# Performance work log

Hardware: AMD Instinct MI355X
Metric: run time of the kernel (lower is better)

The kernel has to match this reference:

```python
import jax, jax.numpy as jnp
import numpy as np

B, H, S, DH = 1, 16, 4096, 64
SPARSITY = 0.1
NEG = -1e9


def setup_inputs() -> dict:
    key = jax.random.key(0)
    kq, kk, kv, kp, km = jax.random.split(key, 5)
    query = jax.random.normal(kq, (B, H, S, DH), dtype=jnp.float32)
    k_ = jax.random.normal(kk, (B, H, S, DH), dtype=jnp.float32)
    v_ = jax.random.normal(kv, (B, H, S, DH), dtype=jnp.float32)
    pat = jax.random.uniform(kp, (S, S)) < SPARSITY
    pat = pat | jnp.eye(S, dtype=bool)
    sparse_pattern = pat[None, None]  # [1,1,S,S]
    mask = jax.random.randint(km, (1, 1, 1, S), 0, 2, dtype=jnp.int32)
    return {"query": query, "key": k_, "value": v_,
            "sparse_pattern": sparse_pattern, "mask": mask}


def reference(query, key, value, sparse_pattern, mask):
    scale = 1.0 / jnp.sqrt(jnp.asarray(DH, dtype=query.dtype))
    # [B,H,S,S] attention scores
    scores = jnp.einsum('bhqd,bhkd->bhqk', query, key) * scale
    scores = jnp.where(sparse_pattern, scores, NEG)
    scores = jnp.where(mask == 0, NEG, scores)
    weights = jax.nn.softmax(scores, axis=-1)
    return jnp.einsum('bhqk,bhkd->bhqd', weights, value)
```

## Files before the change

### kernel.cpp

```cpp
#include <hip/hip_runtime.h>
#include <hip/hip_bf16.h>

#define S_LEN 4096
#define DHD   64
#define NH    16
#define NKT   64
#define KVB   64
#define WQ    32
#define NW    4
#define QB    (WQ * NW)
#define QSCALE 0.18033688011112042f
#define THRS   8.656170245333781f

typedef __bf16 bf16x8 __attribute__((ext_vector_type(8)));
typedef __bf16 bf16x4 __attribute__((ext_vector_type(4)));
typedef float  f32x16 __attribute__((ext_vector_type(16)));
typedef float  f32x4  __attribute__((ext_vector_type(4)));
typedef unsigned u32;
typedef unsigned u32x4v __attribute__((ext_vector_type(4)));
typedef unsigned long long u64;

#define MFMA32 __builtin_amdgcn_mfma_f32_32x32x16_bf16

__device__ __forceinline__ float fexp2(float x) {
  float r;
  asm("v_exp_f32 %0, %1" : "=v"(r) : "v"(x));
  return r;
}
#define EXP2(x) fexp2(x)

__device__ __forceinline__ int swz(int row, int col) {
  return row * 64 + ((((col >> 3) ^ (row & 7)) << 3) | (col & 7));
}

__device__ __forceinline__ u32 pk(float a, float b) {
  __bf16 x = (__bf16)a, y = (__bf16)b;
  u32 lo = (u32)__builtin_bit_cast(unsigned short, x);
  u32 hi = (u32)__builtin_bit_cast(unsigned short, y);
  return lo | (hi << 16);
}

__device__ __forceinline__ void gload16(const void* g, void* l) {
  __builtin_amdgcn_global_load_lds((const __attribute__((address_space(1))) void*)g,
                                   (__attribute__((address_space(3))) void*)l, 16, 0, 0);
}

__device__ __forceinline__ void plswap(u32& x, u32& y) {
  asm("v_permlane32_swap_b32 %0, %1" : "+v"(x), "+v"(y));
}

union PAW { u32x4v w; bf16x8 h; };

template <int MODE>
__device__ __forceinline__ bool patget(const void* __restrict__ p, int q, int k) {
  const size_t idx = (size_t)q * S_LEN + k;
  if constexpr (MODE == 1) return ((const unsigned char*)p)[idx] != 0;
  else if constexpr (MODE == 0) return ((const int*)p)[idx] != 0;
  else return ((const float*)p)[idx] != 0.0f;
}

__global__ void __launch_bounds__(256, 2) attn32c(
    const float* __restrict__ Qg, const __bf16* __restrict__ Kc, const __bf16* __restrict__ Vc,
    const u64* __restrict__ packw,
    const int* __restrict__ mask, float* __restrict__ out) {
  __shared__ __align__(16) __bf16 Kls[4][KVB * DHD];
  __shared__ __align__(16) __bf16 Vls[4][DHD * KVB];
  __shared__ float sfb[NW][WQ];
  __shared__ int msum[NW];

  const int gid = (blockIdx.x & 7) * 64 + (blockIdx.x >> 3);
  const int h = gid >> 5;
  const int q0 = (gid & 31) * QB;

  const int t = threadIdx.x, lane = t & 63, wv = t >> 6;
  const int l32 = lane & 31, hi = lane >> 5;
  const int qrow = q0 + wv * WQ + l32;

  int c = 0;
#pragma unroll
  for (int j = 0; j < 16; j++) c += (mask[t * 16 + j] != 0);
#pragma unroll
  for (int d = 1; d < 64; d <<= 1) c += __shfl_xor(c, d);
  if (lane == 0) msum[wv] = c;

  bf16x8 aQ[4];
  {
    const float* qp = Qg + ((size_t)h * S_LEN + qrow) * DHD;
#pragma unroll
    for (int cc = 0; cc < 4; cc++) {
      float4 x = *(const float4*)(qp + cc * 16 + hi * 8);
      float4 y = *(const float4*)(qp + cc * 16 + hi * 8 + 4);
      bf16x8 f;
      f[0] = (__bf16)(x.x * QSCALE); f[1] = (__bf16)(x.y * QSCALE);
      f[2] = (__bf16)(x.z * QSCALE); f[3] = (__bf16)(x.w * QSCALE);
      f[4] = (__bf16)(y.x * QSCALE); f[5] = (__bf16)(y.y * QSCALE);
      f[6] = (__bf16)(y.z * QSCALE); f[7] = (__bf16)(y.w * QSCALE);
      aQ[cc] = f;
    }
  }
  bf16x8 onesf;
#pragma unroll
  for (int j = 0; j < 8; j++) onesf[j] = (__bf16)1.0f;
  f32x16 zv;
#pragma unroll
  for (int r = 0; r < 16; r++) zv[r] = 0.f;

  __syncthreads();
  const int nact = msum[0] + msum[1] + msum[2] + msum[3];
  const int nt = (nact + 63) >> 6;
  const int np = ((nt + 1) & ~1) >> 1;

  const __bf16* Kb = Kc + (size_t)h * NKT * 4096;
  const __bf16* Vb = Vc + (size_t)h * NKT * 4096;

  auto stage = [&](int slot, int kt) {
    const __bf16* kbase = Kb + (size_t)kt * 4096;
    const __bf16* vbase = Vb + (size_t)kt * 4096;
#pragma unroll
    for (int i = 0; i < 2; i++) {
      const int j = wv * 2 + i;
      gload16(kbase + j * 512 + lane * 8, &Kls[slot][j * 512]);
      gload16(vbase + j * 512 + lane * 8, &Vls[slot][j * 512]);
    }
  };

  f32x16 Oc0 = zv, Oc1 = zv, Ol = zv;
  float m_run = -__builtin_inff();
  const u64* prow = packw + qrow;

  __builtin_amdgcn_sched_barrier(0);
  u64 pwA = prow[0];
  u64 pwB = prow[(size_t)1 * S_LEN];
  stage(0, 0);
  stage(1, 1);

  for (int it = 0; it < np; it++) {
    const int buf = (it & 1) << 1;
    u64 pwA_n = 0, pwB_n = 0;
    if (it + 1 < np) {
      pwA_n = prow[(size_t)(2 * it + 2) * S_LEN];
      pwB_n = prow[(size_t)(2 * it + 3) * S_LEN];
      stage(buf ^ 2, 2 * it + 2);
      stage((buf ^ 2) + 1, 2 * it + 3);
      asm volatile("s_waitcnt vmcnt(10)" ::: "memory");
    } else {
      asm volatile("s_waitcnt vmcnt(0)" ::: "memory");
    }
    __builtin_amdgcn_s_barrier();
    __builtin_amdgcn_sched_barrier(0);

    const __bf16* KlA = Kls[buf];
    const __bf16* KlB = Kls[buf + 1];
    const __bf16* VlA = Vls[buf];
    const __bf16* VlB = Vls[buf + 1];

    f32x16 pA0, pA1, pB0, pB1;
    __builtin_amdgcn_s_setprio(1);
#pragma unroll
    for (int cc = 0; cc < 4; cc++) {
      const int g = (((2 * cc + hi) ^ (l32 & 7)) << 3);
      const bf16x8 kA0 = *(const bf16x8*)&KlA[l32 * 64 + g];
      const bf16x8 kA1 = *(const bf16x8*)&KlA[(32 + l32) * 64 + g];
      const bf16x8 kB0 = *(const bf16x8*)&KlB[l32 * 64 + g];
      const bf16x8 kB1 = *(const bf16x8*)&KlB[(32 + l32) * 64 + g];
      pA0 = MFMA32(kA0, aQ[cc], cc ? pA0 : zv, 0, 0, 0);
      pA1 = MFMA32(kA1, aQ[cc], cc ? pA1 : zv, 0, 0, 0);
      pB0 = MFMA32(kB0, aQ[cc], cc ? pB0 : zv, 0, 0, 0);
      pB1 = MFMA32(kB1, aQ[cc], cc ? pB1 : zv, 0, 0, 0);
    }
    __builtin_amdgcn_s_setprio(0);

    float mx[32];
#pragma unroll
    for (int i = 0; i < 8; i++) {
      mx[i]      = fmaxf(pA0[2 * i], pA0[2 * i + 1]);
      mx[8 + i]  = fmaxf(pA1[2 * i], pA1[2 * i + 1]);
      mx[16 + i] = fmaxf(pB0[2 * i], pB0[2 * i + 1]);
      mx[24 + i] = fmaxf(pB1[2 * i], pB1[2 * i + 1]);
    }
#pragma unroll
    for (int s = 16; s >= 1; s >>= 1)
#pragma unroll
      for (int i = 0; i < s; i++) mx[i] = fmaxf(mx[i], mx[i + s]);
    const float pm = fmaxf(mx[0], __shfl_xor(mx[0], 32));

    if (!__all(pm <= m_run + THRS)) {
      const float mn = fmaxf(m_run, pm);
      const float sf = EXP2(m_run - mn);
      m_run = mn;
      if (lane < 32) sfb[wv][l32] = sf;
#pragma unroll
      for (int rq = 0; rq < 4; rq++) {
        const f32x4 s4 = *(const f32x4*)&sfb[wv][rq * 8 + 4 * hi];
#pragma unroll
        for (int rr = 0; rr < 4; rr++) {
          Oc0[rq * 4 + rr] *= s4[rr];
          Oc1[rq * 4 + rr] *= s4[rr];
          Ol[rq * 4 + rr]  *= s4[rr];
        }
      }
    }

    const u32 a0b = (u32)pwA, a1b = (u32)(pwA >> 32);
    const u32 wA0 = hi ? ((a0b >> 4) | (a1b << 28)) : a0b;
    const u32 wA1 = hi ? (a1b >> 4) : a1b;
    const u32 b0b = (u32)pwB, b1b = (u32)(pwB >> 32);
    const u32 wB0 = hi ? ((b0b >> 4) | (b1b << 28)) : b0b;
    const u32 wB1 = hi ? (b1b >> 4) : b1b;

#pragma unroll
    for (int r = 0; r < 16; r++) {
      const int sp = (r & 3) + 8 * (r >> 2);
      float eA0 = EXP2(pA0[r] - m_run);
      float eA1 = EXP2(pA1[r] - m_run);
      float eB0 = EXP2(pB0[r] - m_run);
      float eB1 = EXP2(pB1[r] - m_run);
      const int tA0 = (int)(wA0 << (31 - sp)) >> 31;
      const int tA1 = (int)(wA1 << (31 - sp)) >> 31;
      const int tB0 = (int)(wB0 << (31 - sp)) >> 31;
      const int tB1 = (int)(wB1 << (31 - sp)) >> 31;
      pA0[r] = __uint_as_float(__float_as_uint(eA0) & (u32)tA0);
      pA1[r] = __uint_as_float(__float_as_uint(eA1) & (u32)tA1);
      pB0[r] = __uint_as_float(__float_as_uint(eB0) & (u32)tB0);
      pB1[r] = __uint_as_float(__float_as_uint(eB1) & (u32)tB1);
    }

    __builtin_amdgcn_s_setprio(1);
#pragma unroll
    for (int ks = 0; ks < 4; ks++) {
      const f32x16& ps = (ks < 2) ? pA0 : pA1;
      const int b = (ks & 1) * 8;
      u32 x0 = pk(ps[b + 0], ps[b + 1]), x1 = pk(ps[b + 2], ps[b + 3]);
      u32 y0 = pk(ps[b + 4], ps[b + 5]), y1 = pk(ps[b + 6], ps[b + 7]);
      plswap(x0, y0);
      plswap(x1, y1);
      PAW pa;
      pa.w = (u32x4v){x0, x1, y0, y1};
      const int g = (((2 * ks + hi) ^ (l32 & 7)) << 3);
      const bf16x8 v0 = *(const bf16x8*)&VlA[l32 * 64 + g];
      const bf16x8 v1 = *(const bf16x8*)&VlA[(32 + l32) * 64 + g];
      Oc0 = MFMA32(pa.h, v0, Oc0, 0, 0, 0);
      Oc1 = MFMA32(pa.h, v1, Oc1, 0, 0, 0);
      Ol  = MFMA32(pa.h, onesf, Ol, 0, 0, 0);
    }
#pragma unroll
    for (int ks = 0; ks < 4; ks++) {
      const f32x16& ps = (ks < 2) ? pB0 : pB1;
      const int b = (ks & 1) * 8;
      u32 x0 = pk(ps[b + 0], ps[b + 1]), x1 = pk(ps[b + 2], ps[b + 3]);
      u32 y0 = pk(ps[b + 4], ps[b + 5]), y1 = pk(ps[b + 6], ps[b + 7]);
      plswap(x0, y0);
      plswap(x1, y1);
      PAW pa;
      pa.w = (u32x4v){x0, x1, y0, y1};
      const int g = (((2 * ks + hi) ^ (l32 & 7)) << 3);
      const bf16x8 v0 = *(const bf16x8*)&VlB[l32 * 64 + g];
      const bf16x8 v1 = *(const bf16x8*)&VlB[(32 + l32) * 64 + g];
      Oc0 = MFMA32(pa.h, v0, Oc0, 0, 0, 0);
      Oc1 = MFMA32(pa.h, v1, Oc1, 0, 0, 0);
      Ol  = MFMA32(pa.h, onesf, Ol, 0, 0, 0);
    }
    __builtin_amdgcn_s_setprio(0);

    __builtin_amdgcn_s_barrier();
    pwA = pwA_n;
    pwB = pwB_n;
  }

  float* ob = out + ((size_t)h * S_LEN + q0 + wv * WQ) * DHD;
#pragma unroll
  for (int rq = 0; rq < 4; rq++) {
#pragma unroll
    for (int rr = 0; rr < 4; rr++) {
      const int r = rq * 4 + rr;
      const float linv = 1.0f / Ol[r];
      const int qq = rr + 8 * rq + 4 * hi;
      ob[(size_t)qq * DHD + l32]      = Oc0[r] * linv;
      ob[(size_t)qq * DHD + 32 + l32] = Oc1[r] * linv;
    }
  }
}

__global__ void __launch_bounds__(256) prep_all(
    const unsigned* __restrict__ pat32, const int* __restrict__ mask,
    const float* __restrict__ K, const float* __restrict__ V,
    u64* __restrict__ packw, __bf16* __restrict__ Kc, __bf16* __restrict__ Vc) {
  __shared__ int idxs[S_LEN];
  __shared__ int red8[8];
  __shared__ __align__(16) unsigned rowbuf[4096];
  const int t = threadIdx.x, lane = t & 63, wv = t >> 6;

  unsigned mb = 0;
#pragma unroll
  for (int j = 0; j < 16; j++) mb |= (unsigned)(mask[t * 16 + j] != 0) << j;
  const int cnt = __builtin_popcount(mb);
  int inc = cnt;
  for (int d = 1; d < 64; d <<= 1) {
    const int v = __shfl_up(inc, d);
    if (lane >= d) inc += v;
  }
  if (lane == 63) red8[wv] = inc;
  __syncthreads();
  int base = 0;
  for (int w = 0; w < wv; w++) base += red8[w];
  const int nact = red8[0] + red8[1] + red8[2] + red8[3];
  int pfx = base + inc - cnt;
#pragma unroll
  for (int j = 0; j < 16; j++)
    if ((mb >> j) & 1) idxs[pfx++] = t * 16 + j;
  __syncthreads();
  const int nt = (nact + 63) >> 6;
  const int nte = (nt + 1) & ~1;

  if (blockIdx.x < S_LEN) {
    const int q = blockIdx.x;
    unsigned acc = 0;
    for (int i = t; i < 4096; i += 256) {
      const unsigned w = pat32[i];
      if (w == 0x3F800000u) acc |= 2u;
      else if (w & 0xFFFFFF00u) acc |= 1u;
    }
    for (int d = 1; d < 64; d <<= 1) acc |= (unsigned)__shfl_xor((int)acc, d);
    if (lane == 0) red8[4 + wv] = (int)acc;
    __syncthreads();
    acc = (unsigned)(red8[4] | red8[5] | red8[6] | red8[7]);
    const int mode = (acc & 2u) ? 2 : ((acc & 1u) ? 1 : 0);

    if (mode == 1) {
      const uint4* src = (const uint4*)((const unsigned char*)pat32 + ((size_t)q << 12));
      ((uint4*)rowbuf)[t] = src[t];
    } else {
      const uint4* src = (const uint4*)(pat32 + ((size_t)q << 12));
#pragma unroll
      for (int i = 0; i < 4; i++) ((uint4*)rowbuf)[t + 256 * i] = src[t + 256 * i];
    }
    __syncthreads();
    const unsigned char* rb = (const unsigned char*)rowbuf;
    const int nkw = nte * 64;
    for (int bs = 0; bs < nkw; bs += 256) {
      const int j = bs + t;
      bool pb = false;
      if (j < nact) {
        const int k = idxs[j];
        pb = (mode == 1) ? (rb[k] != 0) : (rowbuf[k] != 0);
      }
      const u64 b = __ballot(pb);
      if ((t & 63) == 0) packw[(size_t)(j >> 6) * S_LEN + q] = b;
    }
  } else {
    const int bb = blockIdx.x - S_LEN;
    const int kt = bb & 63, h = bb >> 6;
    if (kt >= nte) return;
    __bf16* Kd = Kc + ((size_t)(h * NKT + kt)) * 4096;
    __bf16* Vd = Vc + ((size_t)(h * NKT + kt)) * 4096;
    const float* Kb = K + (size_t)h * S_LEN * DHD;
    const float* Vb = V + (size_t)h * S_LEN * DHD;
#pragma unroll
    for (int i = 0; i < 4; i++) {
      const int u = t + 256 * i;
      const int kk = u >> 4, d = (u & 15) * 4;
      const int kg = kt * 64 + kk;
      float4 v = {0.f, 0.f, 0.f, 0.f};
      if (kg < nact) v = *(const float4*)(Kb + (size_t)idxs[kg] * DHD + d);
      bf16x4 b;
      b[0] = (__bf16)v.x; b[1] = (__bf16)v.y; b[2] = (__bf16)v.z; b[3] = (__bf16)v.w;
      *(bf16x4*)&Kd[swz(kk, d)] = b;
    }
#pragma unroll
    for (int i = 0; i < 2; i++) {
      const int u = t + 256 * i;
      const int kp = u & 31, d4 = u >> 5;
      const int g0 = kt * 64 + 2 * kp, g1 = g0 + 1;
      float4 a = {0.f, 0.f, 0.f, 0.f}, b = {0.f, 0.f, 0.f, 0.f};
      if (g0 < nact) a = *(const float4*)(Vb + (size_t)idxs[g0] * DHD + d4 * 4);
      if (g1 < nact) b = *(const float4*)(Vb + (size_t)idxs[g1] * DHD + d4 * 4);
      const float* A = reinterpret_cast<const float*>(&a);
      const float* B = reinterpret_cast<const float*>(&b);
#pragma unroll
      for (int j = 0; j < 4; j++) {
        *(u32*)&Vd[swz(d4 * 4 + j, 2 * kp)] = pk(A[j], B[j]);
      }
    }
  }
}

template <bool PACKED, int MODE>
__global__ void __launch_bounds__(256, 2) attn32(
    const float* __restrict__ Qg, const float* __restrict__ Kg, const float* __restrict__ Vg,
    const u64* __restrict__ packw, const void* __restrict__ pat, const int* __restrict__ mask,
    float* __restrict__ out) {
  __shared__ __align__(16) __bf16 Kls[2][KVB * DHD];
  __shared__ __align__(16) __bf16 Vls[2][DHD * KVB];
  __shared__ float sfb[NW][WQ];
  const int gid = (blockIdx.x & 7) * 64 + (blockIdx.x >> 3);
  const int h = gid >> 5;
  const int q0 = (gid & 31) * QB;
  const int t = threadIdx.x, lane = t & 63, wv = t >> 6;
  const int l32 = lane & 31, hi = lane >> 5;
  const int qrow = q0 + wv * WQ + l32;
  bf16x8 aQ[4];
  {
    const float* qp = Qg + ((size_t)h * S_LEN + qrow) * DHD;
#pragma unroll
    for (int cc = 0; cc < 4; cc++) {
      float4 x = *(const float4*)(qp + cc * 16 + hi * 8);
      float4 y = *(const float4*)(qp + cc * 16 + hi * 8 + 4);
      bf16x8 f;
      f[0] = (__bf16)(x.x * QSCALE); f[1] = (__bf16)(x.y * QSCALE);
      f[2] = (__bf16)(x.z * QSCALE); f[3] = (__bf16)(x.w * QSCALE);
      f[4] = (__bf16)(y.x * QSCALE); f[5] = (__bf16)(y.y * QSCALE);
      f[6] = (__bf16)(y.z * QSCALE); f[7] = (__bf16)(y.w * QSCALE);
      aQ[cc] = f;
    }
  }
  const float* Kb = Kg + (size_t)h * S_LEN * DHD;
  const float* Vb = Vg + (size_t)h * S_LEN * DHD;
  float4 kreg[4], vreg0[2], vreg1[2];
  auto issue_loads = [&](int kt) {
    const float* kbase = Kb + (size_t)kt * KVB * DHD;
    const float* vbase = Vb + (size_t)kt * KVB * DHD;
#pragma unroll
    for (int i = 0; i < 4; i++) {
      const int u = t + 256 * i;
      kreg[i] = *(const float4*)(kbase + (size_t)(u >> 4) * DHD + (u & 15) * 4);
    }
#pragma unroll
    for (int i = 0; i < 2; i++) {
      const int u = t + 256 * i;
      const int kp = u & 31, d4 = u >> 5;
      vreg0[i] = *(const float4*)(vbase + (size_t)(2 * kp) * DHD + d4 * 4);
      vreg1[i] = *(const float4*)(vbase + (size_t)(2 * kp + 1) * DHD + d4 * 4);
    }
  };
  auto write_tile = [&](int buf) {
    __bf16* Kd = Kls[buf];
    __bf16* Vd = Vls[buf];
#pragma unroll
    for (int i = 0; i < 4; i++) {
      const int u = t + 256 * i;
      const int kk = u >> 4, d = (u & 15) * 4;
      const float4 v = kreg[i];
      bf16x4 b;
      b[0] = (__bf16)v.x; b[1] = (__bf16)v.y; b[2] = (__bf16)v.z; b[3] = (__bf16)v.w;
      *(bf16x4*)&Kd[swz(kk, d)] = b;
    }
#pragma unroll
    for (int i = 0; i < 2; i++) {
      const int u = t + 256 * i;
      const int kp = u & 31, d4 = u >> 5;
      const float* A = reinterpret_cast<const float*>(&vreg0[i]);
      const float* B = reinterpret_cast<const float*>(&vreg1[i]);
#pragma unroll
      for (int j = 0; j < 4; j++) {
        *(u32*)&Vd[swz(d4 * 4 + j, 2 * kp)] = pk(A[j], B[j]);
      }
    }
  };
  f32x16 Oc0, Oc1;
#pragma unroll
  for (int r = 0; r < 16; r++) { Oc0[r] = 0.f; Oc1[r] = 0.f; }
  float m_run = -__builtin_inff(), l_run = 0.f;
  const u64* prow = PACKED ? (packw + qrow) : nullptr;
  issue_loads(0);
  write_tile(0);
  __syncthreads();
  int cur = 0;
  for (int kt = 0; kt < NKT; kt++) {
    if (kt + 1 < NKT) issue_loads(kt + 1);
    u64 pw;
    if constexpr (PACKED) {
      pw = prow[(size_t)kt * S_LEN];
    } else {
      pw = 0;
      for (int j = 0; j < 64; j++) {
        const bool pb = patget<MODE>(pat, qrow, kt * 64 + j) && (mask[kt * 64 + j] != 0);
        pw |= (u64)pb << j;
      }
    }
    const __bf16* Kl = Kls[cur];
    f32x16 p0, p1;
#pragma unroll
    for (int r = 0; r < 16; r++) { p0[r] = 0.f; p1[r] = 0.f; }
#pragma unroll
    for (int cc = 0; cc < 4; cc++) {
      const int g = (((2 * cc + hi) ^ (l32 & 7)) << 3);
      const bf16x8 k0 = *(const bf16x8*)&Kl[l32 * 64 + g];
      const bf16x8 k1 = *(const bf16x8*)&Kl[(32 + l32) * 64 + g];
      p0 = MFMA32(k0, aQ[cc], p0, 0, 0, 0);
      p1 = MFMA32(k1, aQ[cc], p1, 0, 0, 0);
    }
    float pm = p0[0];
#pragma unroll
    for (int r = 1; r < 16; r++) pm = fmaxf(pm, p0[r]);
#pragma unroll
    for (int r = 0; r < 16; r++) pm = fmaxf(pm, p1[r]);
    pm = fmaxf(pm, __shfl_xor(pm, 32));
    if (!__all(pm <= m_run + THRS)) {
      const float mn = fmaxf(m_run, pm);
      const float sf = EXP2(m_run - mn);
      m_run = mn;
      l_run *= sf;
      if (lane < 32) sfb[wv][l32] = sf;
#pragma unroll
      for (int rq = 0; rq < 4; rq++) {
        const f32x4 s4 = *(const f32x4*)&sfb[wv][rq * 8 + 4 * hi];
#pragma unroll
        for (int rr = 0; rr < 4; rr++) {
          Oc0[rq * 4 + rr] *= s4[rr];
          Oc1[rq * 4 + rr] *= s4[rr];
        }
      }
    }
    const u32 b0 = (u32)pw, b1 = (u32)(pw >> 32);
    const u32 w0 = hi ? ((b0 >> 4) | (b1 << 28)) : b0;
    const u32 w1 = hi ? (b1 >> 4) : b1;
    float ls = 0.f;
#pragma unroll
    for (int r = 0; r < 16; r++) {
      const int sp = (r & 3) + 8 * (r >> 2);
      float e0 = EXP2(p0[r] - m_run);
      float e1 = EXP2(p1[r] - m_run);
      const int t0 = (int)(w0 << (31 - sp)) >> 31;
      const int t1 = (int)(w1 << (31 - sp)) >> 31;
      e0 = __uint_as_float(__float_as_uint(e0) & (u32)t0);
      e1 = __uint_as_float(__float_as_uint(e1) & (u32)t1);
      p0[r] = e0; p1[r] = e1;
      ls += e0 + e1;
    }
    ls += __shfl_xor(ls, 32);
    l_run += ls;
    const __bf16* Vl = Vls[cur];
#pragma unroll
    for (int ks = 0; ks < 4; ks++) {
      const f32x16& ps = (ks < 2) ? p0 : p1;
      const int b = (ks & 1) * 8;
      u32 x0 = pk(ps[b + 0], ps[b + 1]), x1 = pk(ps[b + 2], ps[b + 3]);
      u32 y0 = pk(ps[b + 4], ps[b + 5]), y1 = pk(ps[b + 6], ps[b + 7]);
      plswap(x0, y0);
      plswap(x1, y1);
      PAW pa;
      pa.w = (u32x4v){x0, x1, y0, y1};
      const int g = (((2 * ks + hi) ^ (l32 & 7)) << 3);
      const bf16x8 v0 = *(const bf16x8*)&Vl[l32 * 64 + g];
      const bf16x8 v1 = *(const bf16x8*)&Vl[(32 + l32) * 64 + g];
      Oc0 = MFMA32(pa.h, v0, Oc0, 0, 0, 0);
      Oc1 = MFMA32(pa.h, v1, Oc1, 0, 0, 0);
    }
    if (kt + 1 < NKT) write_tile(cur ^ 1);
    __syncthreads();
    cur ^= 1;
  }
  const float linv = 1.0f / l_run;
  if (lane < 32) sfb[wv][l32] = linv;
  __syncthreads();
  float* ob = out + ((size_t)h * S_LEN + q0 + wv * WQ) * DHD;
#pragma unroll
  for (int rq = 0; rq < 4; rq++) {
    const f32x4 s4 = *(const f32x4*)&sfb[wv][rq * 8 + 4 * hi];
#pragma unroll
    for (int rr = 0; rr < 4; rr++) {
      const int r = rq * 4 + rr;
      const int qq = rr + 8 * rq + 4 * hi;
      ob[(size_t)qq * DHD + l32]      = Oc0[r] * s4[rr];
      ob[(size_t)qq * DHD + 32 + l32] = Oc1[r] * s4[rr];
    }
  }
}

__global__ void detect_kernel(const unsigned* __restrict__ p, int* __restrict__ flag) {
  __shared__ unsigned red[256];
  const int t = threadIdx.x;
  unsigned acc = 0;
  for (int i = t; i < 16384; i += 256) {
    const unsigned w = p[i];
    if (w == 0x3F800000u) acc |= 2u;
    else if (w & 0xFFFFFF00u) acc |= 1u;
  }
  red[t] = acc;
  __syncthreads();
  if (t == 0) {
    unsigned a = 0;
    for (int i = 0; i < 256; i++) a |= red[i];
    flag[0] = (a & 2u) ? 2 : ((a & 1u) ? 1 : 0);
  }
}

__global__ void pack_mask_kernel(const int* __restrict__ mask, u64* __restrict__ maskw) {
  const int w = threadIdx.x;
  u64 m = 0;
  for (int j = 0; j < 64; j++) m |= (u64)(mask[(w << 6) + j] != 0) << j;
  maskw[w] = m;
}

__global__ void pack_pat_kernel(const void* __restrict__ pat, const u64* __restrict__ maskw,
                                u64* __restrict__ packw, const int* __restrict__ flagp) {
  const int gid = blockIdx.x * 256 + threadIdx.x;
  const int q = gid >> 6, w = gid & 63;
  const int mode = flagp[0];
  u64 bits = 0;
  if (mode == 1) {
    const u64* p = (const u64*)((const unsigned char*)pat + ((size_t)q << 12) + (w << 6));
#pragma unroll
    for (int c = 0; c < 8; c++) {
      u64 v = p[c];
      v |= v >> 4; v |= v >> 2; v |= v >> 1;
      v &= 0x0101010101010101ull;
      bits |= ((v * 0x0102040810204080ull) >> 56) << (c * 8);
    }
  } else if (mode == 0) {
    const int4* p = (const int4*)((const int*)pat + ((size_t)q << 12) + ((size_t)w << 6));
#pragma unroll
    for (int c = 0; c < 16; c++) {
      const int4 x = p[c];
      bits |= (u64)(x.x != 0) << (c * 4);
      bits |= (u64)(x.y != 0) << (c * 4 + 1);
      bits |= (u64)(x.z != 0) << (c * 4 + 2);
      bits |= (u64)(x.w != 0) << (c * 4 + 3);
    }
  } else {
    const float4* p = (const float4*)((const float*)pat + ((size_t)q << 12) + ((size_t)w << 6));
#pragma unroll
    for (int c = 0; c < 16; c++) {
      const float4 x = p[c];
      bits |= (u64)(x.x != 0.0f) << (c * 4);
      bits |= (u64)(x.y != 0.0f) << (c * 4 + 1);
      bits |= (u64)(x.z != 0.0f) << (c * 4 + 2);
      bits |= (u64)(x.w != 0.0f) << (c * 4 + 3);
    }
  }
  packw[(size_t)w * S_LEN + q] = bits & maskw[w];
}

extern "C" void kernel_launch(void* const* d_in, const int* in_sizes, int n_in,
                              void* d_out, int out_size, void* d_ws, size_t ws_size,
                              hipStream_t stream) {
  (void)in_sizes; (void)n_in; (void)out_size;
  const float* Q  = (const float*)d_in[0];
  const float* K  = (const float*)d_in[1];
  const float* V  = (const float*)d_in[2];
  const void* pat = d_in[3];
  const int* mask = (const int*)d_in[4];
  float* out      = (float*)d_out;

  const size_t FLAG_OFF  = 0;
  const size_t MASKW_OFF = 24576;
  const size_t PACKW_OFF = 32768;
  const size_t KC_OFF    = PACKW_OFF + (size_t)S_LEN * NKT * 8;
  const size_t VC_OFF    = KC_OFF + (size_t)NH * NKT * 4096 * 2;
  const size_t NEED_FULL = VC_OFF + (size_t)NH * NKT * 4096 * 2;
  const size_t NEED_MID  = PACKW_OFF + (size_t)S_LEN * NKT * 8;

  const dim3 grid(32 * NH, 1);

  if (ws_size >= NEED_FULL) {
    u64* packw = (u64*)((char*)d_ws + PACKW_OFF);
    __bf16* Kc = (__bf16*)((char*)d_ws + KC_OFF);
    __bf16* Vc = (__bf16*)((char*)d_ws + VC_OFF);
    prep_all<<<S_LEN + NKT * NH, 256, 0, stream>>>((const unsigned*)pat, mask, K, V,
                                                   packw, Kc, Vc);
    attn32c<<<grid, 256, 0, stream>>>(Q, Kc, Vc, packw, mask, out);
  } else if (ws_size >= NEED_MID) {
    int* flag  = (int*)((char*)d_ws + FLAG_OFF);
    u64* maskw = (u64*)((char*)d_ws + MASKW_OFF);
    u64* packw = (u64*)((char*)d_ws + PACKW_OFF);
    detect_kernel<<<1, 256, 0, stream>>>((const unsigned*)pat, flag);
    pack_mask_kernel<<<1, 64, 0, stream>>>(mask, maskw);
    pack_pat_kernel<<<(S_LEN * 64) / 256, 256, 0, stream>>>(pat, maskw, packw, flag);
    attn32<true, 0><<<grid, 256, 0, stream>>>(Q, K, V, packw, pat, mask, out);
  } else {
    attn32<false, 1><<<grid, 256, 0, stream>>>(Q, K, V, nullptr, pat, mask, out);
  }
}
```

Measured before the change: 94.78 us.

## Split KV range across two workgroups per query block and merge partials

Adds a split-K (flash-decoding style) path: each query block's compacted KV tiles are split between two workgroups, doubling the grid to 1024 and raising the occupancy target to 4 waves-groups per CU with a smaller double-buffered LDS. Partial outputs, row maxima and sums are written to workspace, then a separate merge kernel combines them with rescaling. This targets underfilled CUs with only 512 workgroups. The cost is extra global traffic for the partials, one more launch, and the loss of the two-tile-per-iteration pipelining. The mid-workspace fallback path is also removed.

New measurement: 130.5 us. +37.7%, slower.

```diff
diff --git a/kernel.cpp b/kernel.cpp
--- a/kernel.cpp
+++ b/kernel.cpp
@@ -59,18 +59,21 @@
   else return ((const float*)p)[idx] != 0.0f;
 }
 
-__global__ void __launch_bounds__(256, 2) attn32c(
+__global__ void __launch_bounds__(256, 4) attn32s(
     const float* __restrict__ Qg, const __bf16* __restrict__ Kc, const __bf16* __restrict__ Vc,
-    const u64* __restrict__ packw,
-    const int* __restrict__ mask, float* __restrict__ out) {
-  __shared__ __align__(16) __bf16 Kls[4][KVB * DHD];
-  __shared__ __align__(16) __bf16 Vls[4][DHD * KVB];
+    const u64* __restrict__ packw, const int* __restrict__ mask,
+    float* __restrict__ O0, float* __restrict__ Opart,
+    float* __restrict__ l0a, float* __restrict__ m0a,
+    float* __restrict__ l1a, float* __restrict__ m1a) {
+  __shared__ __align__(16) __bf16 Kls[2][KVB * DHD];
+  __shared__ __align__(16) __bf16 Vls[2][DHD * KVB];
   __shared__ float sfb[NW][WQ];
   __shared__ int msum[NW];
 
-  const int gid = (blockIdx.x & 7) * 64 + (blockIdx.x >> 3);
-  const int h = gid >> 5;
-  const int q0 = (gid & 31) * QB;
+  const int wgid = (blockIdx.x & 7) * 128 + (blockIdx.x >> 3);
+  const int h = wgid >> 6;
+  const int q0 = ((wgid >> 1) & 31) * QB;
+  const int split = wgid & 1;
 
   const int t = threadIdx.x, lane = t & 63, wv = t >> 6;
   const int l32 = lane & 31, hi = lane >> 5;
@@ -108,11 +111,217 @@
   __syncthreads();
   const int nact = msum[0] + msum[1] + msum[2] + msum[3];
   const int nt = (nact + 63) >> 6;
-  const int np = ((nt + 1) & ~1) >> 1;
+  const int nh0 = (nt + 1) >> 1;
+  const int t0 = split ? nh0 : 0;
+  const int t1 = split ? nt : nh0;
 
   const __bf16* Kb = Kc + (size_t)h * NKT * 4096;
   const __bf16* Vb = Vc + (size_t)h * NKT * 4096;
 
+  auto stage = [&](int buf, int kt) {
+    const __bf16* kbase = Kb + (size_t)kt * 4096;
+    const __bf16* vbase = Vb + (size_t)kt * 4096;
+#pragma unroll
+    for (int i = 0; i < 2; i++) {
+      const int j = wv * 2 + i;
+      gload16(kbase + j * 512 + lane * 8, &Kls[buf][j * 512]);
+      gload16(vbase + j * 512 + lane * 8, &Vls[buf][j * 512]);
+    }
+  };
+
+  f32x16 Oc0 = zv, Oc1 = zv, Ol = zv;
+  float m_run = -__builtin_inff();
+  const u64* prow = packw + qrow;
+
+  __builtin_amdgcn_sched_barrier(0);
+  u64 pw = 0, pw_n = 0;
+  int cur = 0;
+  if (t0 < t1) {
+    pw = prow[(size_t)t0 * S_LEN];
+    stage(0, t0);
+  }
+
+  for (int kt = t0; kt < t1; kt++) {
+    if (kt + 1 < t1) {
+      pw_n = prow[(size_t)(kt + 1) * S_LEN];
+      stage(cur ^ 1, kt + 1);
+      asm volatile("s_waitcnt vmcnt(5)" ::: "memory");
+    } else {
+      asm volatile("s_waitcnt vmcnt(0)" ::: "memory");
+    }
+    __builtin_amdgcn_s_barrier();
+    __builtin_amdgcn_sched_barrier(0);
+
+    const __bf16* Kl = Kls[cur];
+    const __bf16* Vl = Vls[cur];
+
+    f32x16 p0, p1;
+    __builtin_amdgcn_s_setprio(1);
+#pragma unroll
+    for (int cc = 0; cc < 4; cc++) {
+      const int g = (((2 * cc + hi) ^ (l32 & 7)) << 3);
+      const bf16x8 k0 = *(const bf16x8*)&Kl[l32 * 64 + g];
+      const bf16x8 k1 = *(const bf16x8*)&Kl[(32 + l32) * 64 + g];
+      p0 = MFMA32(k0, aQ[cc], cc ? p0 : zv, 0, 0, 0);
+      p1 = MFMA32(k1, aQ[cc], cc ? p1 : zv, 0, 0, 0);
+    }
+    __builtin_amdgcn_s_setprio(0);
+
+    float mx[16];
+#pragma unroll
+    for (int i = 0; i < 8; i++) {
+      mx[i]     = fmaxf(p0[2 * i], p0[2 * i + 1]);
+      mx[8 + i] = fmaxf(p1[2 * i], p1[2 * i + 1]);
+    }
+#pragma unroll
+    for (int s = 8; s >= 1; s >>= 1)
+#pragma unroll
+      for (int i = 0; i < s; i++) mx[i] = fmaxf(mx[i], mx[i + s]);
+    const float pm = fmaxf(mx[0], __shfl_xor(mx[0], 32));
+
+    if (!__all(pm <= m_run + THRS)) {
+      const float mn = fmaxf(m_run, pm);
+      const float sf = EXP2(m_run - mn);
+      m_run = mn;
+      if (lane < 32) sfb[wv][l32] = sf;
+#pragma unroll
+      for (int rq = 0; rq < 4; rq++) {
+        const f32x4 s4 = *(const f32x4*)&sfb[wv][rq * 8 + 4 * hi];
+#pragma unroll
+        for (int rr = 0; rr < 4; rr++) {
+          Oc0[rq * 4 + rr] *= s4[rr];
+          Oc1[rq * 4 + rr] *= s4[rr];
+          Ol[rq * 4 + rr]  *= s4[rr];
+        }
+      }
+    }
+
+    const u32 b0 = (u32)pw, b1 = (u32)(pw >> 32);
+    const u32 w0 = hi ? ((b0 >> 4) | (b1 << 28)) : b0;
+    const u32 w1 = hi ? (b1 >> 4) : b1;
+
+#pragma unroll
+    for (int r = 0; r < 16; r++) {
+      const int sp = (r & 3) + 8 * (r >> 2);
+      float e0 = EXP2(p0[r] - m_run);
+      float e1 = EXP2(p1[r] - m_run);
+      const int tt0 = (int)(w0 << (31 - sp)) >> 31;
+      const int tt1 = (int)(w1 << (31 - sp)) >> 31;
+      p0[r] = __uint_as_float(__float_as_uint(e0) & (u32)tt0);
+      p1[r] = __uint_as_float(__float_as_uint(e1) & (u32)tt1);
+    }
+
+    __builtin_amdgcn_s_setprio(1);
+#pragma unroll
+    for (int ks = 0; ks < 4; ks++) {
+      const f32x16& ps = (ks < 2) ? p0 : p1;
+      const int b = (ks & 1) * 8;
+      u32 x0 = pk(ps[b + 0], ps[b + 1]), x1 = pk(ps[b + 2], ps[b + 3]);
+      u32 y0 = pk(ps[b + 4], ps[b + 5]), y1 = pk(ps[b + 6], ps[b + 7]);
+      plswap(x0, y0);
+      plswap(x1, y1);
+      PAW pa;
+      pa.w = (u32x4v){x0, x1, y0, y1};
+      const int g = (((2 * ks + hi) ^ (l32 & 7)) << 3);
+      const bf16x8 v0 = *(const bf16x8*)&Vl[l32 * 64 + g];
+      const bf16x8 v1 = *(const bf16x8*)&Vl[(32 + l32) * 64 + g];
+      Oc0 = MFMA32(pa.h, v0, Oc0, 0, 0, 0);
+      Oc1 = MFMA32(pa.h, v1, Oc1, 0, 0, 0);
+      Ol  = MFMA32(pa.h, onesf, Ol, 0, 0, 0);
+    }
+    __builtin_amdgcn_s_setprio(0);
+
+    __builtin_amdgcn_s_barrier();
+    cur ^= 1;
+    pw = pw_n;
+  }
+
+  float* Od = split ? Opart : O0;
+  float* lA = split ? l1a : l0a;
+  float* mA = split ? m1a : m0a;
+  const int rb = h * S_LEN + q0 + wv * WQ;
+  if (lane < 32) mA[rb + l32] = m_run;
+  float* ob = Od + (size_t)rb * DHD;
+#pragma unroll
+  for (int rq = 0; rq < 4; rq++) {
+#pragma unroll
+    for (int rr = 0; rr < 4; rr++) {
+      const int r = rq * 4 + rr;
+      const int qq = rr + 8 * rq + 4 * hi;
+      ob[(size_t)qq * DHD + l32]      = Oc0[r];
+      ob[(size_t)qq * DHD + 32 + l32] = Oc1[r];
+      if (l32 == 0) lA[rb + qq] = Ol[r];
+    }
+  }
+}
+
+__global__ void __launch_bounds__(256) merge_k(
+    float* __restrict__ out, const float* __restrict__ Op,
+    const float* __restrict__ l0a, const float* __restrict__ m0a,
+    const float* __restrict__ l1a, const float* __restrict__ m1a) {
+  const int gid = blockIdx.x * 256 + threadIdx.x;
+  const int row = gid >> 4, c4 = (gid & 15) << 2;
+  const float mm0 = m0a[row], mm1 = m1a[row];
+  const float mm = fmaxf(mm0, mm1);
+  const float s0 = EXP2(mm0 - mm), s1 = EXP2(mm1 - mm);
+  const float inv = 1.0f / (l0a[row] * s0 + l1a[row] * s1);
+  float4* op = (float4*)(out + (size_t)row * DHD + c4);
+  const float4 a = *op;
+  const float4 b = *(const float4*)(Op + (size_t)row * DHD + c4);
+  float4 r;
+  r.x = (a.x * s0 + b.x * s1) * inv;
+  r.y = (a.y * s0 + b.y * s1) * inv;
+  r.z = (a.z * s0 + b.z * s1) * inv;
+  r.w = (a.w * s0 + b.w * s1) * inv;
+  *op = r;
+}
+
+__global__ void __launch_bounds__(256, 2) attn32c2(
+    const float* __restrict__ Qg, const __bf16* __restrict__ Kc, const __bf16* __restrict__ Vc,
+    const u64* __restrict__ packw, const int* __restrict__ mask, float* __restrict__ out) {
+  __shared__ __align__(16) __bf16 Kls[4][KVB * DHD];
+  __shared__ __align__(16) __bf16 Vls[4][DHD * KVB];
+  __shared__ float sfb[NW][WQ];
+  __shared__ int msum[NW];
+  const int gid = (blockIdx.x & 7) * 64 + (blockIdx.x >> 3);
+  const int h = gid >> 5;
+  const int q0 = (gid & 31) * QB;
+  const int t = threadIdx.x, lane = t & 63, wv = t >> 6;
+  const int l32 = lane & 31, hi = lane >> 5;
+  const int qrow = q0 + wv * WQ + l32;
+  int c = 0;
+#pragma unroll
+  for (int j = 0; j < 16; j++) c += (mask[t * 16 + j] != 0);
+#pragma unroll
+  for (int d = 1; d < 64; d <<= 1) c += __shfl_xor(c, d);
+  if (lane == 0) msum[wv] = c;
+  bf16x8 aQ[4];
+  {
+    const float* qp = Qg + ((size_t)h * S_LEN + qrow) * DHD;
+#pragma unroll
+    for (int cc = 0; cc < 4; cc++) {
+      float4 x = *(const float4*)(qp + cc * 16 + hi * 8);
+      float4 y = *(const float4*)(qp + cc * 16 + hi * 8 + 4);
+      bf16x8 f;
+      f[0] = (__bf16)(x.x * QSCALE); f[1] = (__bf16)(x.y * QSCALE);
+      f[2] = (__bf16)(x.z * QSCALE); f[3] = (__bf16)(x.w * QSCALE);
+      f[4] = (__bf16)(y.x * QSCALE); f[5] = (__bf16)(y.y * QSCALE);
+      f[6] = (__bf16)(y.z * QSCALE); f[7] = (__bf16)(y.w * QSCALE);
+      aQ[cc] = f;
+    }
+  }
+  bf16x8 onesf;
+#pragma unroll
+  for (int j = 0; j < 8; j++) onesf[j] = (__bf16)1.0f;
+  f32x16 zv;
+#pragma unroll
+  for (int r = 0; r < 16; r++) zv[r] = 0.f;
+  __syncthreads();
+  const int nact = msum[0] + msum[1] + msum[2] + msum[3];
+  const int nt = (nact + 63) >> 6;
+  const int np = ((nt + 1) & ~1) >> 1;
+  const __bf16* Kb = Kc + (size_t)h * NKT * 4096;
+  const __bf16* Vb = Vc + (size_t)h * NKT * 4096;
   auto stage = [&](int slot, int kt) {
     const __bf16* kbase = Kb + (size_t)kt * 4096;
     const __bf16* vbase = Vb + (size_t)kt * 4096;
@@ -123,17 +332,14 @@
       gload16(vbase + j * 512 + lane * 8, &Vls[slot][j * 512]);
     }
   };
-
   f32x16 Oc0 = zv, Oc1 = zv, Ol = zv;
   float m_run = -__builtin_inff();
   const u64* prow = packw + qrow;
-
   __builtin_amdgcn_sched_barrier(0);
   u64 pwA = prow[0];
   u64 pwB = prow[(size_t)1 * S_LEN];
   stage(0, 0);
   stage(1, 1);
-
   for (int it = 0; it < np; it++) {
     const int buf = (it & 1) << 1;
     u64 pwA_n = 0, pwB_n = 0;
@@ -148,12 +354,10 @@
     }
     __builtin_amdgcn_s_barrier();
     __builtin_amdgcn_sched_barrier(0);
-
     const __bf16* KlA = Kls[buf];
     const __bf16* KlB = Kls[buf + 1];
     const __bf16* VlA = Vls[buf];
     const __bf16* VlB = Vls[buf + 1];
-
     f32x16 pA0, pA1, pB0, pB1;
     __builtin_amdgcn_s_setprio(1);
 #pragma unroll
@@ -169,7 +373,6 @@
       pB1 = MFMA32(kB1, aQ[cc], cc ? pB1 : zv, 0, 0, 0);
     }
     __builtin_amdgcn_s_setprio(0);
-
     float mx[32];
 #pragma unroll
     for (int i = 0; i < 8; i++) {
@@ -183,7 +386,6 @@
 #pragma unroll
       for (int i = 0; i < s; i++) mx[i] = fmaxf(mx[i], mx[i + s]);
     const float pm = fmaxf(mx[0], __shfl_xor(mx[0], 32));
-
     if (!__all(pm <= m_run + THRS)) {
       const float mn = fmaxf(m_run, pm);
       const float sf = EXP2(m_run - mn);
@@ -200,14 +402,12 @@
         }
       }
     }
-
     const u32 a0b = (u32)pwA, a1b = (u32)(pwA >> 32);
     const u32 wA0 = hi ? ((a0b >> 4) | (a1b << 28)) : a0b;
     const u32 wA1 = hi ? (a1b >> 4) : a1b;
     const u32 b0b = (u32)pwB, b1b = (u32)(pwB >> 32);
     const u32 wB0 = hi ? ((b0b >> 4) | (b1b << 28)) : b0b;
     const u32 wB1 = hi ? (b1b >> 4) : b1b;
-
 #pragma unroll
     for (int r = 0; r < 16; r++) {
       const int sp = (r & 3) + 8 * (r >> 2);
@@ -224,7 +424,6 @@
       pB0[r] = __uint_as_float(__float_as_uint(eB0) & (u32)tB0);
       pB1[r] = __uint_as_float(__float_as_uint(eB1) & (u32)tB1);
     }
-
     __builtin_amdgcn_s_setprio(1);
 #pragma unroll
     for (int ks = 0; ks < 4; ks++) {
@@ -261,12 +460,10 @@
       Ol  = MFMA32(pa.h, onesf, Ol, 0, 0, 0);
     }
     __builtin_amdgcn_s_setprio(0);
-
     __builtin_amdgcn_s_barrier();
     pwA = pwA_n;
     pwB = pwB_n;
   }
-
   float* ob = out + ((size_t)h * S_LEN + q0 + wv * WQ) * DHD;
 #pragma unroll
   for (int rq = 0; rq < 4; rq++) {
@@ -384,11 +581,10 @@
   }
 }
 
-template <bool PACKED, int MODE>
+template <int MODE>
 __global__ void __launch_bounds__(256, 2) attn32(
     const float* __restrict__ Qg, const float* __restrict__ Kg, const float* __restrict__ Vg,
-    const u64* __restrict__ packw, const void* __restrict__ pat, const int* __restrict__ mask,
-    float* __restrict__ out) {
+    const void* __restrict__ pat, const int* __restrict__ mask, float* __restrict__ out) {
   __shared__ __align__(16) __bf16 Kls[2][KVB * DHD];
   __shared__ __align__(16) __bf16 Vls[2][DHD * KVB];
   __shared__ float sfb[NW][WQ];
@@ -460,22 +656,16 @@
 #pragma unroll
   for (int r = 0; r < 16; r++) { Oc0[r] = 0.f; Oc1[r] = 0.f; }
   float m_run = -__builtin_inff(), l_run = 0.f;
-  const u64* prow = PACKED ? (packw + qrow) : nullptr;
   issue_loads(0);
   write_tile(0);
   __syncthreads();
   int cur = 0;
   for (int kt = 0; kt < NKT; kt++) {
     if (kt + 1 < NKT) issue_loads(kt + 1);
-    u64 pw;
-    if constexpr (PACKED) {
-      pw = prow[(size_t)kt * S_LEN];
-    } else {
-      pw = 0;
-      for (int j = 0; j < 64; j++) {
-        const bool pb = patget<MODE>(pat, qrow, kt * 64 + j) && (mask[kt * 64 + j] != 0);
-        pw |= (u64)pb << j;
-      }
+    u64 pw = 0;
+    for (int j = 0; j < 64; j++) {
+      const bool pb = patget<MODE>(pat, qrow, kt * 64 + j) && (mask[kt * 64 + j] != 0);
+      pw |= (u64)pb << j;
     }
     const __bf16* Kl = Kls[cur];
     f32x16 p0, p1;
@@ -567,70 +757,6 @@
   }
 }
 
-__global__ void detect_kernel(const unsigned* __restrict__ p, int* __restrict__ flag) {
-  __shared__ unsigned red[256];
-  const int t = threadIdx.x;
-  unsigned acc = 0;
-  for (int i = t; i < 16384; i += 256) {
-    const unsigned w = p[i];
-    if (w == 0x3F800000u) acc |= 2u;
-    else if (w & 0xFFFFFF00u) acc |= 1u;
-  }
-  red[t] = acc;
-  __syncthreads();
-  if (t == 0) {
-    unsigned a = 0;
-    for (int i = 0; i < 256; i++) a |= red[i];
-    flag[0] = (a & 2u) ? 2 : ((a & 1u) ? 1 : 0);
-  }
-}
-
-__global__ void pack_mask_kernel(const int* __restrict__ mask, u64* __restrict__ maskw) {
-  const int w = threadIdx.x;
-  u64 m = 0;
-  for (int j = 0; j < 64; j++) m |= (u64)(mask[(w << 6) + j] != 0) << j;
-  maskw[w] = m;
-}
-
-__global__ void pack_pat_kernel(const void* __restrict__ pat, const u64* __restrict__ maskw,
-                                u64* __restrict__ packw, const int* __restrict__ flagp) {
-  const int gid = blockIdx.x * 256 + threadIdx.x;
-  const int q = gid >> 6, w = gid & 63;
-  const int mode = flagp[0];
-  u64 bits = 0;
-  if (mode == 1) {
-    const u64* p = (const u64*)((const unsigned char*)pat + ((size_t)q << 12) + (w << 6));
-#pragma unroll
-    for (int c = 0; c < 8; c++) {
-      u64 v = p[c];
-      v |= v >> 4; v |= v >> 2; v |= v >> 1;
-      v &= 0x0101010101010101ull;
-      bits |= ((v * 0x0102040810204080ull) >> 56) << (c * 8);
-    }
-  } else if (mode == 0) {
-    const int4* p = (const int4*)((const int*)pat + ((size_t)q << 12) + ((size_t)w << 6));
-#pragma unroll
-    for (int c = 0; c < 16; c++) {
-      const int4 x = p[c];
-      bits |= (u64)(x.x != 0) << (c * 4);
-      bits |= (u64)(x.y != 0) << (c * 4 + 1);
-      bits |= (u64)(x.z != 0) << (c * 4 + 2);
-      bits |= (u64)(x.w != 0) << (c * 4 + 3);
-    }
-  } else {
-    const float4* p = (const float4*)((const float*)pat + ((size_t)q << 12) + ((size_t)w << 6));
-#pragma unroll
-    for (int c = 0; c < 16; c++) {
-      const float4 x = p[c];
-      bits |= (u64)(x.x != 0.0f) << (c * 4);
-      bits |= (u64)(x.y != 0.0f) << (c * 4 + 1);
-      bits |= (u64)(x.z != 0.0f) << (c * 4 + 2);
-      bits |= (u64)(x.w != 0.0f) << (c * 4 + 3);
-    }
-  }
-  packw[(size_t)w * S_LEN + q] = bits & maskw[w];
-}
-
 extern "C" void kernel_launch(void* const* d_in, const int* in_sizes, int n_in,
                               void* d_out, int out_size, void* d_ws, size_t ws_size,
                               hipStream_t stream) {
@@ -642,32 +768,39 @@
   const int* mask = (const int*)d_in[4];
   float* out      = (float*)d_out;
 
-  const size_t FLAG_OFF  = 0;
-  const size_t MASKW_OFF = 24576;
   const size_t PACKW_OFF = 32768;
   const size_t KC_OFF    = PACKW_OFF + (size_t)S_LEN * NKT * 8;
   const size_t VC_OFF    = KC_OFF + (size_t)NH * NKT * 4096 * 2;
   const size_t NEED_FULL = VC_OFF + (size_t)NH * NKT * 4096 * 2;
-  const size_t NEED_MID  = PACKW_OFF + (size_t)S_LEN * NKT * 8;
-
-  const dim3 grid(32 * NH, 1);
-
-  if (ws_size >= NEED_FULL) {
+  const size_t OPART_OFF = NEED_FULL;
+  const size_t L0_OFF    = OPART_OFF + (size_t)NH * S_LEN * DHD * 4;
+  const size_t M0_OFF    = L0_OFF + (size_t)NH * S_LEN * 4;
+  const size_t L1_OFF    = M0_OFF + (size_t)NH * S_LEN * 4;
+  const size_t M1_OFF    = L1_OFF + (size_t)NH * S_LEN * 4;
+  const size_t NEED_SPLIT = M1_OFF + (size_t)NH * S_LEN * 4;
+
+  if (ws_size >= NEED_SPLIT) {
+    u64* packw = (u64*)((char*)d_ws + PACKW_OFF);
+    __bf16* Kc = (__bf16*)((char*)d_ws + KC_OFF);
+    __bf16* Vc = (__bf16*)((char*)d_ws + VC_OFF);
+    float* Opart = (float*)((char*)d_ws + OPART_OFF);
+    float* l0a = (float*)((char*)d_ws + L0_OFF);
+    float* m0a = (float*)((char*)d_ws + M0_OFF);
+    float* l1a = (float*)((char*)d_ws + L1_OFF);
+    float* m1a = (float*)((char*)d_ws + M1_OFF);
+    prep_all<<<S_LEN + NKT * NH, 256, 0, stream>>>((const unsigned*)pat, mask, K, V,
+                                                   packw, Kc, Vc);
+    attn32s<<<1024, 256, 0, stream>>>(Q, Kc, Vc, packw, mask,
+                                      out, Opart, l0a, m0a, l1a, m1a);
+    merge_k<<<(NH * S_LEN * 16) / 256, 256, 0, stream>>>(out, Opart, l0a, m0a, l1a, m1a);
+  } else if (ws_size >= NEED_FULL) {
     u64* packw = (u64*)((char*)d_ws + PACKW_OFF);
     __bf16* Kc = (__bf16*)((char*)d_ws + KC_OFF);
     __bf16* Vc = (__bf16*)((char*)d_ws + VC_OFF);
     prep_all<<<S_LEN + NKT * NH, 256, 0, stream>>>((const unsigned*)pat, mask, K, V,
                                                    packw, Kc, Vc);
-    attn32c<<<grid, 256, 0, stream>>>(Q, Kc, Vc, packw, mask, out);
-  } else if (ws_size >= NEED_MID) {
-    int* flag  = (int*)((char*)d_ws + FLAG_OFF);
-    u64* maskw = (u64*)((char*)d_ws + MASKW_OFF);
-    u64* packw = (u64*)((char*)d_ws + PACKW_OFF);
-    detect_kernel<<<1, 256, 0, stream>>>((const unsigned*)pat, flag);
-    pack_mask_kernel<<<1, 64, 0, stream>>>(mask, maskw);
-    pack_pat_kernel<<<(S_LEN * 64) / 256, 256, 0, stream>>>(pat, maskw, packw, flag);
-    attn32<true, 0><<<grid, 256, 0, stream>>>(Q, K, V, packw, pat, mask, out);
+    attn32c2<<<dim3(32 * NH), 256, 0, stream>>>(Q, Kc, Vc, packw, mask, out);
   } else {
-    attn32<false, 1><<<grid, 256, 0, stream>>>(Q, K, V, nullptr, pat, mask, out);
-  }
-}
+    attn32<1><<<dim3(32 * NH), 256, 0, stream>>>(Q, K, V, pat, mask, out);
+  }
+}
```
